# Kernel optimization log

Hardware: AMD Instinct MI355X
Metric: run time of the kernel (lower is better)

The kernel has to match this reference:

```python
import jax, jax.numpy as jnp
import numpy as np

NUM_EMBEDDINGS = 16384
EMBEDDING_DIM = 256
B, C, H, W = 8, 256, 32, 32


def _l2_normalize(x, axis=-1, eps=1e-12):
    # matches torch.nn.functional.normalize(p=2): x / max(||x||, eps)
    n = jnp.sqrt(jnp.sum(x * x, axis=axis, keepdims=True))
    return x / jnp.maximum(n, eps)


def setup_inputs() -> dict:
    key = jax.random.key(0)
    k1, k2 = jax.random.split(key)
    z = jax.random.normal(k1, (B, C, H, W), dtype=jnp.float32)
    embedding_weight = jax.random.normal(k2, (NUM_EMBEDDINGS, EMBEDDING_DIM), dtype=jnp.float32)
    return {"z": z, "embedding_weight": embedding_weight}


def reference(z, embedding_weight):
    batch_size, channels, height, width = z.shape
    # [B,C,H,W] -> [B,H,W,C] -> [N, D]
    z_flat = jnp.transpose(z, (0, 2, 3, 1)).reshape(-1, EMBEDDING_DIM)
    z_flat = _l2_normalize(z_flat)                 # l2_norm=True
    emb = _l2_normalize(embedding_weight)
    # squared distances: ||z||^2 + ||e||^2 - 2 z e^T  -> [N, K]
    d = (jnp.sum(z_flat * z_flat, axis=1, keepdims=True)
         + jnp.sum(emb * emb, axis=1)
         - 2.0 * jnp.matmul(z_flat, emb.T))
    indices = jnp.argmin(d, axis=1)                # [N]
    z_q = emb[indices].reshape(batch_size, height, width, EMBEDDING_DIM)
    z_q = jnp.transpose(z_q, (0, 3, 1, 2))         # [B,C,H,W]
    indices = indices.reshape(batch_size, height, width)
    return z_q, indices
```

## Files before the change

### kernel.cpp

```cpp
#include <hip/hip_runtime.h>

#define NUM_E   16384
#define DIM     256
#define NROWS   8192
#define HW      1024
#define BM      128
#define BN      256
#define BK      32
#define NCB     (NUM_E / BN)
#define GATE    2.5e-3f
#define TAUC    2.5e-3f
#define EHID    2.5e-3
#define MAXC    16

#define SWZ(r) ((((r) >> 1) ^ ((r) >> 3)) & 3)

typedef __bf16 bf16x8 __attribute__((ext_vector_type(8)));
typedef float  f32x4  __attribute__((ext_vector_type(4)));
typedef float  f32x16 __attribute__((ext_vector_type(16)));

__device__ __forceinline__ unsigned short f2bf(float x) {
    unsigned u = __float_as_uint(x);
    unsigned r = (u + 0x7fffu + ((u >> 16) & 1u)) >> 16;
    return (unsigned short)r;
}
__device__ __forceinline__ void async_copy16(const void* g, void* l) {
    __builtin_amdgcn_global_load_lds(
        (const __attribute__((address_space(1))) unsigned int*)g,
        (__attribute__((address_space(3))) unsigned int*)l, 16, 0, 0);
}
__device__ __forceinline__ int imax(int a, int b) { return a > b ? a : b; }
__device__ __forceinline__ int imin(int a, int b) { return a < b ? a : b; }

__global__ void k_sumz(const float* __restrict__ z, float* __restrict__ zpart) {
    int n = blockIdx.x * 256 + threadIdx.x;
    int b = n >> 10, hw = n & 1023;
    int cb = blockIdx.y;
    const float* p = z + (size_t)(b * DIM + cb * 16) * HW + hw;
    float s = 0.f;
    #pragma unroll
    for (int c = 0; c < 16; c++) { float v = p[c * HW]; s += v * v; }
    zpart[cb * NROWS + n] = s;
}

__global__ void k_prep_z(const float* __restrict__ z, const float* __restrict__ zpart,
                         unsigned short* __restrict__ Zh) {
    __shared__ float T[64 * 68];
    __shared__ __align__(16) float Tinv[64];
    int t = threadIdx.x;
    int n0 = blockIdx.x * 64, c0 = blockIdx.y * 64;
    int b = n0 >> 10, hw0 = n0 & 1023;
    if (t < 64) {
        float s = 0.f;
        #pragma unroll
        for (int cb = 0; cb < 16; cb++) s += zpart[cb * NROWS + n0 + t];
        Tinv[t] = 1.0f / fmaxf(sqrtf(s), 1e-12f);
    }
    __syncthreads();
    #pragma unroll
    for (int i = 0; i < 4; i++) {
        int f = t + 256 * i;
        int cc = f >> 4, n4 = (f & 15) * 4;
        float4 v  = *(const float4*)(z + (size_t)(b * DIM + c0 + cc) * HW + hw0 + n4);
        float4 iv = *(const float4*)&Tinv[n4];
        v.x *= iv.x; v.y *= iv.y; v.z *= iv.z; v.w *= iv.w;
        *(float4*)&T[cc * 68 + n4] = v;
    }
    __syncthreads();
    #pragma unroll
    for (int i = 0; i < 4; i++) {
        int f = t + 256 * i;
        int nn = f >> 4, c4 = (f & 15) * 4;
        ushort4 h;
        h.x = f2bf(T[(c4+0)*68 + nn]);
        h.y = f2bf(T[(c4+1)*68 + nn]);
        h.z = f2bf(T[(c4+2)*68 + nn]);
        h.w = f2bf(T[(c4+3)*68 + nn]);
        *(ushort4*)(Zh + (size_t)(n0 + nn) * DIM + c0 + c4) = h;
    }
}

__global__ void k_prep_e(const float* __restrict__ emb, float* __restrict__ inv_e,
                         double* __restrict__ se2, unsigned short* __restrict__ Eh,
                         int* __restrict__ cnt, int* __restrict__ cnt2) {
    if (blockIdx.x == 0 && threadIdx.x == 0) { *cnt = 0; *cnt2 = 0; }
    int wv = threadIdx.x >> 6, lane = threadIdx.x & 63;
    int k = blockIdx.x * 4 + wv;
    float4 v = *(const float4*)(emb + (size_t)k * DIM + lane * 4);
    double sq = (double)v.x*v.x + (double)v.y*v.y + (double)v.z*v.z + (double)v.w*v.w;
    for (int off = 32; off > 0; off >>= 1) sq += __shfl_down(sq, off);
    double tot = fmax(__shfl(sq, 0), 1e-24);
    if (lane == 0) { se2[k] = tot; inv_e[k] = 1.0f / fmaxf((float)sqrt(tot), 1e-12f); }
    float s = 1.0f / fmaxf((float)sqrt(tot), 1e-12f);
    ushort4 h;
    h.x = f2bf(v.x * s); h.y = f2bf(v.y * s); h.z = f2bf(v.z * s); h.w = f2bf(v.w * s);
    *(ushort4*)(Eh + (size_t)k * DIM + lane * 4) = h;
}

__launch_bounds__(256, 2)
__global__ void k_score(const unsigned short* __restrict__ Zh,
                        const unsigned short* __restrict__ Eh, f32x4* __restrict__ part) {
    __shared__ __align__(16) int smem[18432];
    unsigned short* lds = (unsigned short*)smem;
    int* kv = smem;
    const int t = threadIdx.x, l = t & 63, w = t >> 6;
    const int wm = w >> 1, wn = w & 1;
    const int m0 = blockIdx.x * BM;
    const int nb = blockIdx.y * BN;
    const int l31 = l & 31, lh = l >> 5;
    const int sr = l >> 2, sp = l & 3;

    const unsigned short* gA0 = Zh + (size_t)m0 * DIM;
    const unsigned short* gB0 = Eh + (size_t)nb * DIM;

    f32x16 acc[2][4];
    #pragma unroll
    for (int i = 0; i < 2; i++)
        #pragma unroll
        for (int j = 0; j < 4; j++) acc[i][j] = (f32x16)0.f;

    auto stage = [&](int dbase, int kc) {
        #pragma unroll
        for (int h = 0; h < 2; h++) {
            int sub = 4 * h + w;
            int r = sub * 16 + sr;
            int c = sp ^ SWZ(r);
            async_copy16(gA0 + (size_t)r * DIM + kc + c * 8, &lds[dbase + sub * 512]);
        }
        #pragma unroll
        for (int h = 0; h < 4; h++) {
            int sub = 4 * h + w;
            int r = sub * 16 + sr;
            int c = sp ^ SWZ(r);
            async_copy16(gB0 + (size_t)r * DIM + kc + c * 8, &lds[dbase + 4096 + sub * 512]);
        }
    };

    stage(0, 0);
    stage(12288, BK);
    for (int kt = 0; kt < DIM / BK; kt++) {
        const int base = (kt % 3) * 12288;
        if (kt < DIM / BK - 1) asm volatile("s_waitcnt vmcnt(6)" ::: "memory");
        else                   asm volatile("s_waitcnt vmcnt(0)" ::: "memory");
        __builtin_amdgcn_s_barrier();
        asm volatile("" ::: "memory");
        bf16x8 ah[2][2], bh[2][4];
        #pragma unroll
        for (int s = 0; s < 2; s++) {
            int c = 2 * s + lh;
            #pragma unroll
            for (int i = 0; i < 2; i++) {
                int r = wm * 64 + i * 32 + l31;
                ah[s][i] = *(const bf16x8*)&lds[base + r * 32 + ((c ^ SWZ(r)) * 8)];
            }
            #pragma unroll
            for (int j = 0; j < 4; j++) {
                int r = wn * 128 + j * 32 + l31;
                bh[s][j] = *(const bf16x8*)&lds[base + 4096 + r * 32 + ((c ^ SWZ(r)) * 8)];
            }
        }
        if (kt + 2 < DIM / BK) stage(((kt + 2) % 3) * 12288, (kt + 2) * BK);
        __builtin_amdgcn_s_setprio(1);
        #pragma unroll
        for (int s = 0; s < 2; s++)
            #pragma unroll
            for (int i = 0; i < 2; i++)
                #pragma unroll
                for (int j = 0; j < 4; j++)
                    acc[i][j] = __builtin_amdgcn_mfma_f32_32x32x16_bf16(ah[s][i], bh[s][j], acc[i][j], 0, 0, 0);
        __builtin_amdgcn_s_setprio(0);
    }
    __syncthreads();

    const int colbase = wn * 128 + l31;
    int KA1 = 0, KA2 = 0, KB1 = 0, KB2 = 0;
    const int rl = t >> 2, q = t & 3;
    #pragma unroll
    for (int i = 0; i < 2; i++) {
        #pragma unroll
        for (int reg = 0; reg < 16; reg++) {
            int k0 = (__float_as_int(acc[i][0][reg] + 2.0f) & 0xFFFFFF00) | colbase;
            int k1 = (__float_as_int(acc[i][1][reg] + 2.0f) & 0xFFFFFF00) | (colbase + 32);
            int k2 = (__float_as_int(acc[i][2][reg] + 2.0f) & 0xFFFFFF00) | (colbase + 64);
            int k3 = (__float_as_int(acc[i][3][reg] + 2.0f) & 0xFFFFFF00) | (colbase + 96);
            int a = imax(k0, k1), b = imin(k0, k1);
            int c = imax(k2, k3), d = imin(k2, k3);
            int K1 = imax(a, c);
            int K2 = imax(imin(a, c), imax(b, d));
            int rr = wm * 32 + (reg & 3) + 8 * (reg >> 2) + 4 * lh;
            int slot = wn * 32 + l31;
            *(int2*)&kv[(rr * 66 + slot) * 2] = make_int2(K1, K2);
        }
        __syncthreads();
        int S1 = 0, S2 = 0;
        const int2* pr = (const int2*)&kv[(rl * 66 + q * 16) * 2];
        #pragma unroll
        for (int u = 0; u < 16; u++) {
            int2 e = pr[u];
            S2 = imax(imax(S2, e.y), imin(S1, e.x));
            S1 = imax(S1, e.x);
        }
        __syncthreads();
        #pragma unroll
        for (int d2 = 1; d2 <= 2; d2 <<= 1) {
            int o1 = __shfl_down(S1, d2), o2 = __shfl_down(S2, d2);
            S2 = imax(imax(S2, o2), imin(S1, o1));
            S1 = imax(S1, o1);
        }
        if (i == 0) { KA1 = S1; KA2 = S2; } else { KB1 = S1; KB2 = S2; }
    }
    if ((t & 3) == 0) {
        int rowA = (rl >> 5) * 64 + (rl & 31);
        int rowB = rowA + 32;
        f32x4 ea;
        ea[0] = __int_as_float(KA1 & 0xFFFFFF00) - 2.0f;
        ea[1] = __int_as_float(nb + (KA1 & 0xFF));
        ea[2] = __int_as_float(KA2 & 0xFFFFFF00) - 2.0f;
        ea[3] = __int_as_float(nb + (KA2 & 0xFF));
        part[(size_t)blockIdx.y * NROWS + m0 + rowA] = ea;
        f32x4 eb;
        eb[0] = __int_as_float(KB1 & 0xFFFFFF00) - 2.0f;
        eb[1] = __int_as_float(nb + (KB1 & 0xFF));
        eb[2] = __int_as_float(KB2 & 0xFFFFFF00) - 2.0f;
        eb[3] = __int_as_float(nb + (KB2 & 0xFF));
        part[(size_t)blockIdx.y * NROWS + m0 + rowB] = eb;
    }
}

__global__ void k_final(const f32x4* __restrict__ part, int* __restrict__ idx_ws,
                        float* __restrict__ out_idx, int* __restrict__ flags,
                        int* __restrict__ cnt, int* __restrict__ cand,
                        int* __restrict__ ccnt, float* __restrict__ v2q) {
    __shared__ f32x4 red[8][32];
    __shared__ float bcV1[32], bcV2[32];
    __shared__ int   lcc[32];
    __shared__ int   lcand[32][MAXC];
    __shared__ float sv2[8][32];
    const int nl = threadIdx.x & 31, sc = threadIdx.x >> 5;
    const int n = blockIdx.x * 32 + nl;
    if (threadIdx.x < 32) lcc[threadIdx.x] = 0;
    float V1 = -2e9f, V2 = -2e9f; int I1 = 0;
    for (int s = sc * 8; s < sc * 8 + 8; s++) {
        f32x4 e = part[(size_t)s * NROWS + n];
        float v1 = e[0]; int i1 = __float_as_int(e[1]); float v2 = e[2];
        V2 = fmaxf(fmaxf(V2, v2), fminf(v1, V1));
        I1 = (v1 > V1) ? i1 : I1;
        V1 = fmaxf(V1, v1);
    }
    f32x4 me; me[0] = V1; me[1] = __int_as_float(I1); me[2] = V2; me[3] = 0.f;
    red[sc][nl] = me;
    __syncthreads();
    if (threadIdx.x < 32) {
        float W1 = -2e9f, W2 = -2e9f; int J1 = 0;
        #pragma unroll
        for (int s2 = 0; s2 < 8; s2++) {
            f32x4 e = red[s2][threadIdx.x];
            float v1 = e[0]; int i1 = __float_as_int(e[1]); float v2 = e[2];
            W2 = fmaxf(fmaxf(W2, v2), fminf(v1, W1));
            J1 = (v1 > W1) ? i1 : J1;
            W1 = fmaxf(W1, v1);
        }
        int nn = blockIdx.x * 32 + threadIdx.x;
        idx_ws[nn] = J1;
        out_idx[nn] = (float)J1;
        bcV1[threadIdx.x] = W1;
        bcV2[threadIdx.x] = W2;
    }
    __syncthreads();
    float thr = bcV1[nl] - TAUC;
    float lv2 = -2e9f;
    for (int s = sc * 8; s < sc * 8 + 8; s++) {
        f32x4 e = part[(size_t)s * NROWS + n];
        if (e[0] >= thr) {
            int pos = atomicAdd(&lcc[nl], 2);
            if (pos < MAXC)     lcand[nl][pos]     = __float_as_int(e[1]);
            if (pos + 1 < MAXC) lcand[nl][pos + 1] = __float_as_int(e[3]);
            lv2 = fmaxf(lv2, e[2]);
        }
    }
    sv2[sc][nl] = lv2;
    __syncthreads();
    if (threadIdx.x < 32) {
        int nn = blockIdx.x * 32 + threadIdx.x;
        float W1 = bcV1[threadIdx.x], W2 = bcV2[threadIdx.x];
        if (W1 - W2 < GATE) {
            float m = -2e9f;
            #pragma unroll
            for (int s2 = 0; s2 < 8; s2++) m = fmaxf(m, sv2[s2][threadIdx.x]);
            int p = atomicAdd(cnt, 1);
            flags[p] = nn;
            ccnt[nn] = lcc[threadIdx.x];
            v2q[nn] = m;
            #pragma unroll
            for (int j = 0; j < MAXC; j++) cand[nn * MAXC + j] = lcand[threadIdx.x][j];
        }
    }
}

__launch_bounds__(256)
__global__ void k_rescan_cand(const int* __restrict__ flags, const int* __restrict__ cnt,
                              const int* __restrict__ cand, const int* __restrict__ ccnt,
                              const float* __restrict__ v2q,
                              const float* __restrict__ z, const float* __restrict__ emb,
                              const double* __restrict__ se2,
                              int* __restrict__ idx_ws, float* __restrict__ out_idx,
                              int* __restrict__ flags2, int* __restrict__ cnt2) {
    __shared__ double zs[DIM];
    __shared__ double wv[4];
    __shared__ int    wi[4];
    const int t = threadIdx.x, l = t & 63, w = t >> 6;
    const int F = *cnt;
    for (int f = blockIdx.x; f < F; f += gridDim.x) {
        int n = flags[f];
        int C = ccnt[n];
        int b = n >> 10, hw = n & 1023;
        __syncthreads();
        zs[t] = (double)z[(size_t)(b * DIM + t) * HW + hw];
        __syncthreads();
        double best = -2e18; int bi = 0x7fffffff;
        if (C <= MAXC) {
            double z0 = zs[l*4], z1 = zs[l*4+1], z2 = zs[l*4+2], z3 = zs[l*4+3];
            for (int cix = w; cix < C; cix += 4) {
                int k = cand[n * MAXC + cix];
                float4 ev = *(const float4*)(emb + (size_t)k * DIM + l * 4);
                double d = z0 * (double)ev.x + z1 * (double)ev.y
                         + z2 * (double)ev.z + z3 * (double)ev.w;
                #pragma unroll
                for (int o = 32; o > 0; o >>= 1) d += __shfl_down(d, o);
                if (l == 0) {
                    double qv = d / sqrt(se2[k]);
                    if (qv > best || (qv == best && k < bi)) { best = qv; bi = k; }
                }
            }
        }
        if (l == 0) { wv[w] = best; wi[w] = bi; }
        __syncthreads();
        if (t == 0) {
            if (C > MAXC) {
                int p = atomicAdd(cnt2, 1); flags2[p] = n;
            } else {
                double B = wv[0]; int BI = wi[0];
                #pragma unroll
                for (int x = 1; x < 4; x++)
                    if (wv[x] > B || (wv[x] == B && wi[x] < BI)) { B = wv[x]; BI = wi[x]; }
                if ((double)v2q[n] >= B - EHID) {
                    int p = atomicAdd(cnt2, 1); flags2[p] = n;
                } else {
                    idx_ws[n] = BI; out_idx[n] = (float)BI;
                }
            }
        }
    }
}

__launch_bounds__(256)
__global__ void k_fullscan_part(const int* __restrict__ flags2, const int* __restrict__ cnt2,
                                const float* __restrict__ z, const float* __restrict__ emb,
                                const double* __restrict__ se2, double2* __restrict__ partial) {
    __shared__ double zs[DIM];
    __shared__ double wv[4];
    __shared__ int    wi[4];
    const int t = threadIdx.x, l = t & 63, w = t >> 6;
    const int W = (*cnt2) * 64;
    for (int item = blockIdx.x; item < W; item += gridDim.x) {
        int f = item >> 6, split = item & 63;
        int n = flags2[f];
        int b = n >> 10, hw = n & 1023;
        __syncthreads();
        zs[t] = (double)z[(size_t)(b * DIM + t) * HW + hw];
        __syncthreads();
        double z0 = zs[l*4], z1 = zs[l*4+1], z2 = zs[l*4+2], z3 = zs[l*4+3];
        double best = -2e18; int bi = 0;
        int kbase = split * 256 + w * 64;
        for (int p = 0; p < 64; p++) {
            int k = kbase + p;
            float4 ev = *(const float4*)(emb + (size_t)k * DIM + l * 4);
            double d = z0 * (double)ev.x + z1 * (double)ev.y
                     + z2 * (double)ev.z + z3 * (double)ev.w;
            #pragma unroll
            for (int o = 32; o > 0; o >>= 1) d += __shfl_down(d, o);
            if (l == 0) {
                double qv = d / sqrt(se2[k]);
                if (qv > best) { best = qv; bi = k; }
            }
        }
        if (l == 0) { wv[w] = best; wi[w] = bi; }
        __syncthreads();
        if (t == 0) {
            double B = wv[0]; int BI = wi[0];
            #pragma unroll
            for (int x = 1; x < 4; x++)
                if (wv[x] > B || (wv[x] == B && wi[x] < BI)) { B = wv[x]; BI = wi[x]; }
            partial[item] = make_double2(B, (double)BI);
        }
        __syncthreads();
    }
}

__global__ void k_fullscan_merge(const int* __restrict__ flags2, const int* __restrict__ cnt2,
                                 const double2* __restrict__ partial,
                                 int* __restrict__ idx_ws, float* __restrict__ out_idx) {
    const int F = *cnt2;
    const int l = threadIdx.x & 63, w = threadIdx.x >> 6;
    for (int f = blockIdx.x * 4 + w; f < F; f += gridDim.x * 4) {
        double2 e = partial[(size_t)f * 64 + l];
        double v = e.x; int i = (int)e.y;
        #pragma unroll
        for (int o = 32; o > 0; o >>= 1) {
            double ov = __shfl_down(v, o);
            int    oi = __shfl_down(i, o);
            if (ov > v || (ov == v && oi < i)) { v = ov; i = oi; }
        }
        if (l == 0) { int n = flags2[f]; idx_ws[n] = i; out_idx[n] = (float)i; }
    }
}

__global__ void k_zq(const int* __restrict__ idx_ws, const float* __restrict__ emb,
                     const float* __restrict__ inv_e, float* __restrict__ zq) {
    int t = threadIdx.x;
    int n = blockIdx.x * 256 + t;
    int b = n >> 10, hw = n & 1023;
    int c0 = blockIdx.y * 32;
    int id = idx_ws[n];
    float s = inv_e[id];
    const float* er = emb + (size_t)id * DIM;
    #pragma unroll
    for (int cc = 0; cc < 32; cc += 4) {
        float4 a = *(const float4*)(er + c0 + cc);
        zq[(size_t)(b * DIM + c0 + cc + 0) * HW + hw] = a.x * s;
        zq[(size_t)(b * DIM + c0 + cc + 1) * HW + hw] = a.y * s;
        zq[(size_t)(b * DIM + c0 + cc + 2) * HW + hw] = a.z * s;
        zq[(size_t)(b * DIM + c0 + cc + 3) * HW + hw] = a.w * s;
    }
}

extern "C" void kernel_launch(void* const* d_in, const int* in_sizes, int n_in,
                              void* d_out, int out_size, void* d_ws, size_t ws_size,
                              hipStream_t stream) {
    const float* z   = (const float*)d_in[0];
    const float* emb = (const float*)d_in[1];

    unsigned short* Zh = (unsigned short*)d_ws;
    unsigned short* Eh = Zh + (size_t)NROWS * DIM;
    float*  inv_e = (float*)(Eh + (size_t)NUM_E * DIM);
    float*  zpart = inv_e + NUM_E;
    int*    idx_ws = (int*)(zpart + 16 * NROWS);
    double* se2   = (double*)(idx_ws + NROWS);
    int*    flags = (int*)(se2 + NUM_E);
    int*    flags2 = flags + NROWS;
    int*    cand  = flags2 + NROWS;
    int*    ccnt  = cand + NROWS * MAXC;
    float*  v2q   = (float*)(ccnt + NROWS);
    int*    cnt   = (int*)(v2q + NROWS);
    int*    cnt2  = cnt + 1;

    float* zq      = (float*)d_out;
    float* out_idx = zq + (size_t)NROWS * DIM;
    f32x4*   part    = (f32x4*)zq;
    double2* partial = (double2*)zq;

    k_sumz   <<<dim3(NROWS / 256, 16), 256, 0, stream>>>(z, zpart);
    k_prep_z <<<dim3(NROWS / 64, DIM / 64), 256, 0, stream>>>(z, zpart, Zh);
    k_prep_e <<<NUM_E / 4, 256, 0, stream>>>(emb, inv_e, se2, Eh, cnt, cnt2);
    k_score  <<<dim3(NROWS / BM, NCB), 256, 0, stream>>>(Zh, Eh, part);
    k_final  <<<NROWS / 32, 256, 0, stream>>>(part, idx_ws, out_idx, flags, cnt,
                                              cand, ccnt, v2q);
    k_rescan_cand  <<<1024, 256, 0, stream>>>(flags, cnt, cand, ccnt, v2q, z, emb,
                                              se2, idx_ws, out_idx, flags2, cnt2);
    k_fullscan_part<<<2048, 256, 0, stream>>>(flags2, cnt2, z, emb, se2, partial);
    k_fullscan_merge<<<64, 256, 0, stream>>>(flags2, cnt2, partial, idx_ws, out_idx);
    k_zq     <<<dim3(NROWS / 256, 8), 256, 0, stream>>>(idx_ws, emb, inv_e, zq);
}
```

Baseline: 187.4 us.

## Shrink score tile, pack partials as int2 keys, fuse norm into z prep

Halves the score kernel's N tile to 128 with three blocks per CU. The accumulator now starts at 2.0 so the offset add disappears. Per-block partials are packed int2 sort keys instead of float4, and k_final reconstructs indices from the slab id plus the low byte. The separate k_sumz kernel is folded into k_prep_z, which now computes row norms itself and loops over all channel chunks. This trades more score blocks and twice as many partial slabs, with lower A-tile reuse, for higher occupancy, one fewer launch and smaller partial records.

```diff
diff --git a/kernel.cpp b/kernel.cpp
--- a/kernel.cpp
+++ b/kernel.cpp
@@ -5,7 +5,7 @@
 #define NROWS   8192
 #define HW      1024
 #define BM      128
-#define BN      256
+#define BN      128
 #define BK      32
 #define NCB     (NUM_E / BN)
 #define GATE    2.5e-3f
@@ -32,51 +32,55 @@
 __device__ __forceinline__ int imax(int a, int b) { return a > b ? a : b; }
 __device__ __forceinline__ int imin(int a, int b) { return a < b ? a : b; }
 
-__global__ void k_sumz(const float* __restrict__ z, float* __restrict__ zpart) {
-    int n = blockIdx.x * 256 + threadIdx.x;
-    int b = n >> 10, hw = n & 1023;
-    int cb = blockIdx.y;
-    const float* p = z + (size_t)(b * DIM + cb * 16) * HW + hw;
-    float s = 0.f;
-    #pragma unroll
-    for (int c = 0; c < 16; c++) { float v = p[c * HW]; s += v * v; }
-    zpart[cb * NROWS + n] = s;
-}
-
-__global__ void k_prep_z(const float* __restrict__ z, const float* __restrict__ zpart,
-                         unsigned short* __restrict__ Zh) {
+__global__ void k_prep_z(const float* __restrict__ z, unsigned short* __restrict__ Zh) {
     __shared__ float T[64 * 68];
+    __shared__ float P[16][68];
     __shared__ __align__(16) float Tinv[64];
     int t = threadIdx.x;
-    int n0 = blockIdx.x * 64, c0 = blockIdx.y * 64;
+    int n0 = blockIdx.x * 64;
     int b = n0 >> 10, hw0 = n0 & 1023;
+    {
+        int cg = t >> 4, h4 = (t & 15) * 4;
+        float4 s4 = make_float4(0.f, 0.f, 0.f, 0.f);
+        const float* pz = z + (size_t)(b * DIM + cg * 16) * HW + hw0 + h4;
+        #pragma unroll
+        for (int cc = 0; cc < 16; cc++) {
+            float4 v = *(const float4*)(pz + (size_t)cc * HW);
+            s4.x += v.x * v.x; s4.y += v.y * v.y; s4.z += v.z * v.z; s4.w += v.w * v.w;
+        }
+        *(float4*)&P[cg][h4] = s4;
+    }
+    __syncthreads();
     if (t < 64) {
         float s = 0.f;
         #pragma unroll
-        for (int cb = 0; cb < 16; cb++) s += zpart[cb * NROWS + n0 + t];
+        for (int cg = 0; cg < 16; cg++) s += P[cg][t];
         Tinv[t] = 1.0f / fmaxf(sqrtf(s), 1e-12f);
     }
     __syncthreads();
-    #pragma unroll
-    for (int i = 0; i < 4; i++) {
-        int f = t + 256 * i;
-        int cc = f >> 4, n4 = (f & 15) * 4;
-        float4 v  = *(const float4*)(z + (size_t)(b * DIM + c0 + cc) * HW + hw0 + n4);
-        float4 iv = *(const float4*)&Tinv[n4];
-        v.x *= iv.x; v.y *= iv.y; v.z *= iv.z; v.w *= iv.w;
-        *(float4*)&T[cc * 68 + n4] = v;
-    }
-    __syncthreads();
-    #pragma unroll
-    for (int i = 0; i < 4; i++) {
-        int f = t + 256 * i;
-        int nn = f >> 4, c4 = (f & 15) * 4;
-        ushort4 h;
-        h.x = f2bf(T[(c4+0)*68 + nn]);
-        h.y = f2bf(T[(c4+1)*68 + nn]);
-        h.z = f2bf(T[(c4+2)*68 + nn]);
-        h.w = f2bf(T[(c4+3)*68 + nn]);
-        *(ushort4*)(Zh + (size_t)(n0 + nn) * DIM + c0 + c4) = h;
+    for (int c0 = 0; c0 < DIM; c0 += 64) {
+        #pragma unroll
+        for (int i = 0; i < 4; i++) {
+            int f = t + 256 * i;
+            int cc = f >> 4, n4 = (f & 15) * 4;
+            float4 v  = *(const float4*)(z + (size_t)(b * DIM + c0 + cc) * HW + hw0 + n4);
+            float4 iv = *(const float4*)&Tinv[n4];
+            v.x *= iv.x; v.y *= iv.y; v.z *= iv.z; v.w *= iv.w;
+            *(float4*)&T[cc * 68 + n4] = v;
+        }
+        __syncthreads();
+        #pragma unroll
+        for (int i = 0; i < 4; i++) {
+            int f = t + 256 * i;
+            int nn = f >> 4, c4 = (f & 15) * 4;
+            ushort4 h;
+            h.x = f2bf(T[(c4+0)*68 + nn]);
+            h.y = f2bf(T[(c4+1)*68 + nn]);
+            h.z = f2bf(T[(c4+2)*68 + nn]);
+            h.w = f2bf(T[(c4+3)*68 + nn]);
+            *(ushort4*)(Zh + (size_t)(n0 + nn) * DIM + c0 + c4) = h;
+        }
+        __syncthreads();
     }
 }
 
@@ -97,10 +101,10 @@
     *(ushort4*)(Eh + (size_t)k * DIM + lane * 4) = h;
 }
 
-__launch_bounds__(256, 2)
+__launch_bounds__(256, 3)
 __global__ void k_score(const unsigned short* __restrict__ Zh,
-                        const unsigned short* __restrict__ Eh, f32x4* __restrict__ part) {
-    __shared__ __align__(16) int smem[18432];
+                        const unsigned short* __restrict__ Eh, int2* __restrict__ part) {
+    __shared__ __align__(16) int smem[12288];
     unsigned short* lds = (unsigned short*)smem;
     int* kv = smem;
     const int t = threadIdx.x, l = t & 63, w = t >> 6;
@@ -113,23 +117,23 @@
     const unsigned short* gA0 = Zh + (size_t)m0 * DIM;
     const unsigned short* gB0 = Eh + (size_t)nb * DIM;
 
-    f32x16 acc[2][4];
+    f32x16 acc[2][2];
     #pragma unroll
     for (int i = 0; i < 2; i++)
         #pragma unroll
-        for (int j = 0; j < 4; j++) acc[i][j] = (f32x16)0.f;
+        for (int j = 0; j < 2; j++) acc[i][j] = (f32x16)2.0f;
 
     auto stage = [&](int dbase, int kc) {
         #pragma unroll
         for (int h = 0; h < 2; h++) {
-            int sub = 4 * h + w;
+            int sub = w * 2 + h;
             int r = sub * 16 + sr;
             int c = sp ^ SWZ(r);
             async_copy16(gA0 + (size_t)r * DIM + kc + c * 8, &lds[dbase + sub * 512]);
         }
         #pragma unroll
-        for (int h = 0; h < 4; h++) {
-            int sub = 4 * h + w;
+        for (int h = 0; h < 2; h++) {
+            int sub = w * 2 + h;
             int r = sub * 16 + sr;
             int c = sp ^ SWZ(r);
             async_copy16(gB0 + (size_t)r * DIM + kc + c * 8, &lds[dbase + 4096 + sub * 512]);
@@ -137,14 +141,14 @@
     };
 
     stage(0, 0);
-    stage(12288, BK);
+    stage(8192, BK);
     for (int kt = 0; kt < DIM / BK; kt++) {
-        const int base = (kt % 3) * 12288;
-        if (kt < DIM / BK - 1) asm volatile("s_waitcnt vmcnt(6)" ::: "memory");
+        const int base = (kt % 3) * 8192;
+        if (kt < DIM / BK - 1) asm volatile("s_waitcnt vmcnt(4)" ::: "memory");
         else                   asm volatile("s_waitcnt vmcnt(0)" ::: "memory");
         __builtin_amdgcn_s_barrier();
         asm volatile("" ::: "memory");
-        bf16x8 ah[2][2], bh[2][4];
+        bf16x8 ah[2][2], bh[2][2];
         #pragma unroll
         for (int s = 0; s < 2; s++) {
             int c = 2 * s + lh;
@@ -154,39 +158,34 @@
                 ah[s][i] = *(const bf16x8*)&lds[base + r * 32 + ((c ^ SWZ(r)) * 8)];
             }
             #pragma unroll
-            for (int j = 0; j < 4; j++) {
-                int r = wn * 128 + j * 32 + l31;
+            for (int j = 0; j < 2; j++) {
+                int r = wn * 64 + j * 32 + l31;
                 bh[s][j] = *(const bf16x8*)&lds[base + 4096 + r * 32 + ((c ^ SWZ(r)) * 8)];
             }
         }
-        if (kt + 2 < DIM / BK) stage(((kt + 2) % 3) * 12288, (kt + 2) * BK);
+        if (kt + 2 < DIM / BK) stage(((kt + 2) % 3) * 8192, (kt + 2) * BK);
         __builtin_amdgcn_s_setprio(1);
         #pragma unroll
         for (int s = 0; s < 2; s++)
             #pragma unroll
             for (int i = 0; i < 2; i++)
                 #pragma unroll
-                for (int j = 0; j < 4; j++)
+                for (int j = 0; j < 2; j++)
                     acc[i][j] = __builtin_amdgcn_mfma_f32_32x32x16_bf16(ah[s][i], bh[s][j], acc[i][j], 0, 0, 0);
         __builtin_amdgcn_s_setprio(0);
     }
     __syncthreads();
 
-    const int colbase = wn * 128 + l31;
+    const int cb0 = wn * 64 + l31;
     int KA1 = 0, KA2 = 0, KB1 = 0, KB2 = 0;
     const int rl = t >> 2, q = t & 3;
     #pragma unroll
     for (int i = 0; i < 2; i++) {
         #pragma unroll
         for (int reg = 0; reg < 16; reg++) {
-            int k0 = (__float_as_int(acc[i][0][reg] + 2.0f) & 0xFFFFFF00) | colbase;
-            int k1 = (__float_as_int(acc[i][1][reg] + 2.0f) & 0xFFFFFF00) | (colbase + 32);
-            int k2 = (__float_as_int(acc[i][2][reg] + 2.0f) & 0xFFFFFF00) | (colbase + 64);
-            int k3 = (__float_as_int(acc[i][3][reg] + 2.0f) & 0xFFFFFF00) | (colbase + 96);
-            int a = imax(k0, k1), b = imin(k0, k1);
-            int c = imax(k2, k3), d = imin(k2, k3);
-            int K1 = imax(a, c);
-            int K2 = imax(imin(a, c), imax(b, d));
+            int k0 = (__float_as_int(acc[i][0][reg]) & 0xFFFFFF00) | cb0;
+            int k1 = (__float_as_int(acc[i][1][reg]) & 0xFFFFFF00) | (cb0 + 32);
+            int K1 = imax(k0, k1), K2 = imin(k0, k1);
             int rr = wm * 32 + (reg & 3) + 8 * (reg >> 2) + 4 * lh;
             int slot = wn * 32 + l31;
             *(int2*)&kv[(rr * 66 + slot) * 2] = make_int2(K1, K2);
@@ -212,85 +211,76 @@
     if ((t & 3) == 0) {
         int rowA = (rl >> 5) * 64 + (rl & 31);
         int rowB = rowA + 32;
-        f32x4 ea;
-        ea[0] = __int_as_float(KA1 & 0xFFFFFF00) - 2.0f;
-        ea[1] = __int_as_float(nb + (KA1 & 0xFF));
-        ea[2] = __int_as_float(KA2 & 0xFFFFFF00) - 2.0f;
-        ea[3] = __int_as_float(nb + (KA2 & 0xFF));
-        part[(size_t)blockIdx.y * NROWS + m0 + rowA] = ea;
-        f32x4 eb;
-        eb[0] = __int_as_float(KB1 & 0xFFFFFF00) - 2.0f;
-        eb[1] = __int_as_float(nb + (KB1 & 0xFF));
-        eb[2] = __int_as_float(KB2 & 0xFFFFFF00) - 2.0f;
-        eb[3] = __int_as_float(nb + (KB2 & 0xFF));
-        part[(size_t)blockIdx.y * NROWS + m0 + rowB] = eb;
-    }
-}
-
-__global__ void k_final(const f32x4* __restrict__ part, int* __restrict__ idx_ws,
+        part[(size_t)blockIdx.y * NROWS + m0 + rowA] = make_int2(KA1, KA2);
+        part[(size_t)blockIdx.y * NROWS + m0 + rowB] = make_int2(KB1, KB2);
+    }
+}
+
+__global__ void k_final(const int2* __restrict__ part, int* __restrict__ idx_ws,
                         float* __restrict__ out_idx, int* __restrict__ flags,
                         int* __restrict__ cnt, int* __restrict__ cand,
                         int* __restrict__ ccnt, float* __restrict__ v2q) {
-    __shared__ f32x4 red[8][32];
-    __shared__ float bcV1[32], bcV2[32];
-    __shared__ int   lcc[32];
-    __shared__ int   lcand[32][MAXC];
-    __shared__ float sv2[8][32];
+    __shared__ int rK1[8][33], rK2[8][33], rS[8][33];
+    __shared__ int bK1[32], bK2[32];
+    __shared__ int lcc[32];
+    __shared__ int lcand[32][MAXC];
+    __shared__ int sv2[8][33];
     const int nl = threadIdx.x & 31, sc = threadIdx.x >> 5;
     const int n = blockIdx.x * 32 + nl;
     if (threadIdx.x < 32) lcc[threadIdx.x] = 0;
-    float V1 = -2e9f, V2 = -2e9f; int I1 = 0;
-    for (int s = sc * 8; s < sc * 8 + 8; s++) {
-        f32x4 e = part[(size_t)s * NROWS + n];
-        float v1 = e[0]; int i1 = __float_as_int(e[1]); float v2 = e[2];
-        V2 = fmaxf(fmaxf(V2, v2), fminf(v1, V1));
-        I1 = (v1 > V1) ? i1 : I1;
-        V1 = fmaxf(V1, v1);
-    }
-    f32x4 me; me[0] = V1; me[1] = __int_as_float(I1); me[2] = V2; me[3] = 0.f;
-    red[sc][nl] = me;
+    int K1 = 0, K2 = 0, S1 = 0;
+    for (int s = sc * 16; s < sc * 16 + 16; s++) {
+        int2 e = part[(size_t)s * NROWS + n];
+        S1 = (e.x > K1) ? s : S1;
+        int nK2 = imax(imin(K1, e.x), imax(K2, e.y));
+        K1 = imax(K1, e.x);
+        K2 = nK2;
+    }
+    rK1[sc][nl] = K1; rK2[sc][nl] = K2; rS[sc][nl] = S1;
     __syncthreads();
     if (threadIdx.x < 32) {
-        float W1 = -2e9f, W2 = -2e9f; int J1 = 0;
+        int W1 = 0, W2 = 0, WS = 0;
         #pragma unroll
         for (int s2 = 0; s2 < 8; s2++) {
-            f32x4 e = red[s2][threadIdx.x];
-            float v1 = e[0]; int i1 = __float_as_int(e[1]); float v2 = e[2];
-            W2 = fmaxf(fmaxf(W2, v2), fminf(v1, W1));
-            J1 = (v1 > W1) ? i1 : J1;
-            W1 = fmaxf(W1, v1);
+            int e1 = rK1[s2][threadIdx.x], e2 = rK2[s2][threadIdx.x];
+            WS = (e1 > W1) ? rS[s2][threadIdx.x] : WS;
+            int nW2 = imax(imin(W1, e1), imax(W2, e2));
+            W1 = imax(W1, e1);
+            W2 = nW2;
         }
         int nn = blockIdx.x * 32 + threadIdx.x;
+        int J1 = WS * BN + (W1 & 0xFF);
         idx_ws[nn] = J1;
         out_idx[nn] = (float)J1;
-        bcV1[threadIdx.x] = W1;
-        bcV2[threadIdx.x] = W2;
-    }
-    __syncthreads();
-    float thr = bcV1[nl] - TAUC;
-    float lv2 = -2e9f;
-    for (int s = sc * 8; s < sc * 8 + 8; s++) {
-        f32x4 e = part[(size_t)s * NROWS + n];
-        if (e[0] >= thr) {
+        bK1[threadIdx.x] = W1;
+        bK2[threadIdx.x] = W2;
+    }
+    __syncthreads();
+    int kthr = __float_as_int(__int_as_float(bK1[nl] & 0xFFFFFF00) - TAUC);
+    int lv2 = 0;
+    for (int s = sc * 16; s < sc * 16 + 16; s++) {
+        int2 e = part[(size_t)s * NROWS + n];
+        if (e.x >= kthr) {
             int pos = atomicAdd(&lcc[nl], 2);
-            if (pos < MAXC)     lcand[nl][pos]     = __float_as_int(e[1]);
-            if (pos + 1 < MAXC) lcand[nl][pos + 1] = __float_as_int(e[3]);
-            lv2 = fmaxf(lv2, e[2]);
+            if (pos < MAXC)     lcand[nl][pos]     = s * BN + (e.x & 0xFF);
+            if (pos + 1 < MAXC) lcand[nl][pos + 1] = s * BN + (e.y & 0xFF);
+            lv2 = imax(lv2, e.y);
         }
     }
     sv2[sc][nl] = lv2;
     __syncthreads();
     if (threadIdx.x < 32) {
         int nn = blockIdx.x * 32 + threadIdx.x;
-        float W1 = bcV1[threadIdx.x], W2 = bcV2[threadIdx.x];
-        if (W1 - W2 < GATE) {
-            float m = -2e9f;
-            #pragma unroll
-            for (int s2 = 0; s2 < 8; s2++) m = fmaxf(m, sv2[s2][threadIdx.x]);
+        float v1 = __int_as_float(bK1[threadIdx.x] & 0xFFFFFF00) - 2.0f;
+        float v2 = __int_as_float(bK2[threadIdx.x] & 0xFFFFFF00) - 2.0f;
+        if (v1 - v2 < GATE) {
+            int m = 0;
+            #pragma unroll
+            for (int s2 = 0; s2 < 8; s2++) m = imax(m, sv2[s2][threadIdx.x]);
             int p = atomicAdd(cnt, 1);
             flags[p] = nn;
             ccnt[nn] = lcc[threadIdx.x];
-            v2q[nn] = m;
+            v2q[nn] = __int_as_float(m & 0xFFFFFF00) - 2.0f;
             #pragma unroll
             for (int j = 0; j < MAXC; j++) cand[nn * MAXC + j] = lcand[threadIdx.x][j];
         }
@@ -456,11 +446,10 @@
 
     float* zq      = (float*)d_out;
     float* out_idx = zq + (size_t)NROWS * DIM;
-    f32x4*   part    = (f32x4*)zq;
+    int2*    part    = (int2*)zq;
     double2* partial = (double2*)zq;
 
-    k_sumz   <<<dim3(NROWS / 256, 16), 256, 0, stream>>>(z, zpart);
-    k_prep_z <<<dim3(NROWS / 64, DIM / 64), 256, 0, stream>>>(z, zpart, Zh);
+    k_prep_z <<<NROWS / 64, 256, 0, stream>>>(z, Zh);
     k_prep_e <<<NUM_E / 4, 256, 0, stream>>>(emb, inv_e, se2, Eh, cnt, cnt2);
     k_score  <<<dim3(NROWS / BM, NCB), 256, 0, stream>>>(Zh, Eh, part);
     k_final  <<<NROWS / 32, 256, 0, stream>>>(part, idx_ws, out_idx, flags, cnt,
```

New measurement: 195.2 us. 4.1% more time.
